# Optimization experiments

Hardware: AMD Instinct MI355X
Metric: run time of the kernel (lower is better)

The kernel has to match this reference:

```python
import jax, jax.numpy as jnp
import numpy as np
import math

D_MODEL = 1024
NUM_HEADS = 16
D_K = D_MODEL // NUM_HEADS
MAX_SEQ_LEN = 2048
THETA = 10000.0
BATCH = 2
SEQ = 2048


def setup_inputs() -> dict:
    key = jax.random.key(0)
    ks = jax.random.split(key, 5)
    std = math.sqrt(2.0 / (D_MODEL + D_MODEL))
    def w(k):
        return jnp.clip(std * jax.random.normal(k, (D_MODEL, D_MODEL), dtype=jnp.float32), -3 * std, 3 * std)
    return {
        "x": jax.random.normal(ks[0], (BATCH, SEQ, D_MODEL), dtype=jnp.float32),
        "token_positions": jnp.arange(SEQ, dtype=jnp.int32),
        "Wq": w(ks[1]),
        "Wk": w(ks[2]),
        "Wv": w(ks[3]),
        "Wo": w(ks[4]),
    }


def _rope_tables():
    inv_freq = 1.0 / THETA ** (jnp.arange(0, D_K, 2, dtype=jnp.float32) / D_K)  # [d_k/2]
    positions = jnp.arange(MAX_SEQ_LEN, dtype=jnp.float32)[:, None]             # [max_seq, 1]
    angles = positions * inv_freq                                               # [max_seq, d_k/2]
    return jnp.cos(angles), jnp.sin(angles)


def _apply_rope(x, cos, sin):
    # x: [..., seq, d_k]; cos/sin: [seq, d_k/2] (broadcast over leading dims)
    x1, x2 = x[..., ::2], x[..., 1::2]
    r1 = x1 * cos - x2 * sin
    r2 = x1 * sin + x2 * cos
    return jnp.stack((r1, r2), axis=-1).reshape(x.shape)


def reference(x, token_positions, Wq, Wk, Wv, Wo):
    B, S, D = x.shape
    def proj(W):
        y = jnp.einsum('bsd,od->bso', x, W)
        return y.reshape(B, S, NUM_HEADS, D_K).transpose(0, 2, 1, 3)  # [B,H,S,dk]
    q, k, v = proj(Wq), proj(Wk), proj(Wv)

    cos_t, sin_t = _rope_tables()
    cos, sin = cos_t[token_positions], sin_t[token_positions]  # [S, d_k/2]
    q = _apply_rope(q, cos, sin)
    k = _apply_rope(k, cos, sin)

    scores = jnp.einsum('bhqd,bhkd->bhqk', q, k) / math.sqrt(D_K)
    causal = jnp.tril(jnp.ones((S, S), dtype=bool))
    scores = jnp.where(causal, scores, -jnp.inf)
    attn = jax.nn.softmax(scores, axis=-1)
    out = jnp.einsum('bhqk,bhkd->bhqd', attn, v)
    out = out.transpose(0, 2, 1, 3).reshape(B, S, D)
    return jnp.einsum('bsd,od->bso', out, Wo)
```

## Files before the change

### kernel.cpp

```cpp
#include <hip/hip_runtime.h>
#include <hip/hip_bf16.h>


typedef __attribute__((ext_vector_type(8))) short short8;
typedef __attribute__((ext_vector_type(4))) float floatx4;

static __device__ __forceinline__ unsigned short f2bf(float f) {
  __hip_bfloat16 h = __float2bfloat16(f);
  return *(unsigned short*)&h;
}

static __device__ __forceinline__ unsigned int pk2bf(float a, float b) {
  unsigned int ua = __float_as_uint(a) + 0x8000u;
  unsigned int ub = __float_as_uint(b) + 0x8000u;
  return __builtin_amdgcn_perm(ub, ua, 0x07060302u);
}

static __device__ __forceinline__ float fexp2(float x) {
  float r;
  asm("v_exp_f32 %0, %1\n\ts_nop 0" : "=v"(r) : "v"(x));
  return r;
}

static __device__ __forceinline__ void gl2lds16(const unsigned short* g,
                                                unsigned short* l) {
  __builtin_amdgcn_global_load_lds(
      (const __attribute__((address_space(1))) void*)g,
      (__attribute__((address_space(3))) void*)l, 16, 0, 0);
}

__global__ __launch_bounds__(256) void cvt_all(
    const float4* __restrict__ x,  const float4* __restrict__ wq,
    const float4* __restrict__ wk, const float4* __restrict__ wv,
    const float4* __restrict__ wo,
    ushort4* __restrict__ xb,  ushort4* __restrict__ wqb,
    ushort4* __restrict__ wkb, ushort4* __restrict__ wvb,
    ushort4* __restrict__ wob,
    const int* __restrict__ tokpos,
    float* __restrict__ ctab, float* __restrict__ stab) {
  int t = blockIdx.y;
  int i = blockIdx.x * 256 + threadIdx.x;
  if (t == 5) {
    if (i < 65536) {
      int s = i >> 5, f = i & 31;
      float inv = expf(-9.210340371976184f * (float)(2 * f) / 64.0f);
      float ang = (float)tokpos[s] * inv;
      ctab[i] = cosf(ang);
      stab[i] = sinf(ang);
    }
    return;
  }
  const float4* s = (t == 0) ? x : (t == 1) ? wq : (t == 2) ? wk : (t == 3) ? wv : wo;
  ushort4* d = (t == 0) ? xb : (t == 1) ? wqb : (t == 2) ? wkb : (t == 3) ? wvb : wob;
  int n4 = (t == 0) ? 1048576 : 262144;
  if (i < n4) {
    float4 v = s[i];
    ushort4 o;
    o.x = f2bf(v.x); o.y = f2bf(v.y); o.z = f2bf(v.z); o.w = f2bf(v.w);
    d[i] = o;
  }
}

__global__ __launch_bounds__(256) void qkv_mfma(
    const unsigned short* __restrict__ X,
    const unsigned short* __restrict__ Wq,
    const unsigned short* __restrict__ Wk,
    const unsigned short* __restrict__ Wv,
    const float* __restrict__ ctab, const float* __restrict__ stab,
    unsigned short* __restrict__ Qo, unsigned short* __restrict__ Ko,
    unsigned short* __restrict__ Vo) {
  int mat = blockIdx.z;
  const unsigned short* W = (mat == 0) ? Wq : ((mat == 1) ? Wk : Wv);
  unsigned short* Out = (mat == 0) ? Qo : ((mat == 1) ? Ko : Vo);
  int t = blockIdx.x + (blockIdx.y << 6);
  int m0 = (t >> 3) * 64, n0 = (t & 7) * 128;

  __shared__ __align__(16) unsigned short lA[2][64 * 64];
  __shared__ __align__(16) unsigned short lB[2][128 * 64];
  int tid = threadIdx.x;
  int wave = tid >> 6, lane = tid & 63;
  int l15 = lane & 15, quad = lane >> 4;
  int rsub = lane >> 3, sch = lane & 7;
  int fsw = l15 & 7;

  floatx4 acc[4][2];
#pragma unroll
  for (int m = 0; m < 4; ++m)
#pragma unroll
    for (int n = 0; n < 2; ++n) acc[m][n] = (floatx4){0.f, 0.f, 0.f, 0.f};

#pragma unroll
  for (int kp = 0; kp < 2; ++kp) {
#pragma unroll
    for (int p = 0; p < 2; ++p) {
      int r = wave * 16 + p * 8 + rsub;
      int g = sch ^ (r & 7);
      gl2lds16(X + (size_t)(m0 + r) * 1024 + kp * 64 + g * 8,
               lA[kp] + (wave * 16 + p * 8) * 64);
    }
#pragma unroll
    for (int p = 0; p < 4; ++p) {
      int r = wave * 32 + p * 8 + rsub;
      int g = sch ^ (r & 7);
      gl2lds16(W + (size_t)(n0 + r) * 1024 + kp * 64 + g * 8,
               lB[kp] + (wave * 32 + p * 8) * 64);
    }
  }
  asm volatile("s_waitcnt vmcnt(6)" ::: "memory");
  __builtin_amdgcn_s_barrier();

  for (int kt = 0; kt < 16; ++kt) {
    int cur = kt & 1;
#pragma unroll
    for (int ks = 0; ks < 2; ++ks) {
      int slot = ((ks * 4 + quad) ^ fsw) * 8;
      short8 af[4], bf[2];
#pragma unroll
      for (int m = 0; m < 4; ++m)
        af[m] = *(const short8*)(lA[cur] + (m * 16 + l15) * 64 + slot);
#pragma unroll
      for (int n = 0; n < 2; ++n)
        bf[n] = *(const short8*)(lB[cur] + (wave * 32 + n * 16 + l15) * 64 + slot);
#pragma unroll
      for (int m = 0; m < 4; ++m)
#pragma unroll
        for (int n = 0; n < 2; ++n)
          acc[m][n] = __builtin_amdgcn_mfma_f32_16x16x32_bf16(
              af[m], bf[n], acc[m][n], 0, 0, 0);
    }
    if (kt == 15) break;
    __builtin_amdgcn_s_barrier();
    if (kt < 14) {
#pragma unroll
      for (int p = 0; p < 2; ++p) {
        int r = wave * 16 + p * 8 + rsub;
        int g = sch ^ (r & 7);
        gl2lds16(X + (size_t)(m0 + r) * 1024 + (kt + 2) * 64 + g * 8,
                 lA[cur] + (wave * 16 + p * 8) * 64);
      }
#pragma unroll
      for (int p = 0; p < 4; ++p) {
        int r = wave * 32 + p * 8 + rsub;
        int g = sch ^ (r & 7);
        gl2lds16(W + (size_t)(n0 + r) * 1024 + (kt + 2) * 64 + g * 8,
                 lB[cur] + (wave * 32 + p * 8) * 64);
      }
      asm volatile("s_waitcnt vmcnt(6)" ::: "memory");
    } else {
      asm volatile("s_waitcnt vmcnt(0)" ::: "memory");
    }
    __builtin_amdgcn_s_barrier();
  }

#pragma unroll
  for (int n = 0; n < 2; ++n) {
    int col = n0 + wave * 32 + n * 16 + l15;
    int h = col >> 6;
    int d = col & 63;
    int pi = d >> 1;
    bool odd = (d & 1) != 0;
    size_t hb = (size_t)h * 2048 * 64;
#pragma unroll
    for (int m = 0; m < 4; ++m) {
      int row0 = m0 + m * 16 + quad * 4;
      int b = row0 >> 11;
      int s0 = row0 & 2047;
      size_t base = (size_t)b * 16 * 2048 * 64 + hb;
      if (mat == 2) {
        ushort4 pv;
        pv.x = f2bf(acc[m][n][0]);
        pv.y = f2bf(acc[m][n][1]);
        pv.z = f2bf(acc[m][n][2]);
        pv.w = f2bf(acc[m][n][3]);
        *(ushort4*)(Out + base + (size_t)d * 2048 + s0) = pv;
      } else {
#pragma unroll
        for (int i = 0; i < 4; ++i) {
          int s = s0 + i;
          float v = acc[m][n][i];
          float p = __shfl_xor(v, 1);
          float c = ctab[s * 32 + pi];
          float sn = stab[s * 32 + pi];
          float res = odd ? fmaf(p, sn, v * c) : fmaf(v, c, -p * sn);
          if (mat == 0) res *= 0.1803368801111204f;
          Out[base + (size_t)s * 64 + d] = f2bf(res);
        }
      }
    }
  }
}

__global__ __launch_bounds__(256) void oproj_mfma(
    const unsigned short* __restrict__ A, const unsigned short* __restrict__ Wo,
    float* __restrict__ Out) {
  __shared__ __align__(16) unsigned short lA[2][64 * 64];
  __shared__ __align__(16) unsigned short lB[2][128 * 64];
  int tid = threadIdx.x;
  int wave = tid >> 6, lane = tid & 63;
  int l15 = lane & 15, quad = lane >> 4;
  int rsub = lane >> 3, sch = lane & 7;
  int fsw = l15 & 7;
  int t = blockIdx.x + (blockIdx.y << 6);
  int m0 = (t >> 3) * 64, n0 = (t & 7) * 128;

  floatx4 acc[4][2];
#pragma unroll
  for (int m = 0; m < 4; ++m)
#pragma unroll
    for (int n = 0; n < 2; ++n) acc[m][n] = (floatx4){0.f, 0.f, 0.f, 0.f};

#pragma unroll
  for (int kp = 0; kp < 2; ++kp) {
#pragma unroll
    for (int p = 0; p < 2; ++p) {
      int r = wave * 16 + p * 8 + rsub;
      int g = sch ^ (r & 7);
      gl2lds16(A + (size_t)(m0 + r) * 1024 + kp * 64 + g * 8,
               lA[kp] + (wave * 16 + p * 8) * 64);
    }
#pragma unroll
    for (int p = 0; p < 4; ++p) {
      int r = wave * 32 + p * 8 + rsub;
      int g = sch ^ (r & 7);
      gl2lds16(Wo + (size_t)(n0 + r) * 1024 + kp * 64 + g * 8,
               lB[kp] + (wave * 32 + p * 8) * 64);
    }
  }
  asm volatile("s_waitcnt vmcnt(6)" ::: "memory");
  __builtin_amdgcn_s_barrier();

  for (int kt = 0; kt < 16; ++kt) {
    int cur = kt & 1;
#pragma unroll
    for (int ks = 0; ks < 2; ++ks) {
      int slot = ((ks * 4 + quad) ^ fsw) * 8;
      short8 af[4], bf[2];
#pragma unroll
      for (int m = 0; m < 4; ++m)
        af[m] = *(const short8*)(lA[cur] + (m * 16 + l15) * 64 + slot);
#pragma unroll
      for (int n = 0; n < 2; ++n)
        bf[n] = *(const short8*)(lB[cur] + (wave * 32 + n * 16 + l15) * 64 + slot);
#pragma unroll
      for (int m = 0; m < 4; ++m)
#pragma unroll
        for (int n = 0; n < 2; ++n)
          acc[m][n] = __builtin_amdgcn_mfma_f32_16x16x32_bf16(
              af[m], bf[n], acc[m][n], 0, 0, 0);
    }
    if (kt == 15) break;
    __builtin_amdgcn_s_barrier();
    if (kt < 14) {
#pragma unroll
      for (int p = 0; p < 2; ++p) {
        int r = wave * 16 + p * 8 + rsub;
        int g = sch ^ (r & 7);
        gl2lds16(A + (size_t)(m0 + r) * 1024 + (kt + 2) * 64 + g * 8,
                 lA[cur] + (wave * 16 + p * 8) * 64);
      }
#pragma unroll
      for (int p = 0; p < 4; ++p) {
        int r = wave * 32 + p * 8 + rsub;
        int g = sch ^ (r & 7);
        gl2lds16(Wo + (size_t)(n0 + r) * 1024 + (kt + 2) * 64 + g * 8,
                 lB[cur] + (wave * 32 + p * 8) * 64);
      }
      asm volatile("s_waitcnt vmcnt(6)" ::: "memory");
    } else {
      asm volatile("s_waitcnt vmcnt(0)" ::: "memory");
    }
    __builtin_amdgcn_s_barrier();
  }

#pragma unroll
  for (int m = 0; m < 4; ++m) {
#pragma unroll
    for (int n = 0; n < 2; ++n) {
      int col = n0 + wave * 32 + n * 16 + l15;
#pragma unroll
      for (int i = 0; i < 4; ++i) {
        int row = m0 + m * 16 + quad * 4 + i;
        Out[(size_t)row * 1024 + col] = acc[m][n][i];
      }
    }
  }
}

static __device__ __forceinline__ void qk_step(
    const unsigned short* lK, int l15, int c0, int c1,
    short8 q0, short8 q1, floatx4 (&sc)[4]) {
#pragma unroll
  for (int sub = 0; sub < 4; ++sub) {
    const unsigned short* kr = lK + (sub * 16 + l15) * 64;
    short8 a0 = *(const short8*)(kr + c0);
    short8 a1 = *(const short8*)(kr + c1);
    floatx4 s = {0.f, 0.f, 0.f, 0.f};
    s = __builtin_amdgcn_mfma_f32_16x16x32_bf16(a0, q0, s, 0, 0, 0);
    s = __builtin_amdgcn_mfma_f32_16x16x32_bf16(a1, q1, s, 0, 0, 0);
    sc[sub] = s;
  }
}

static __device__ __forceinline__ void sm_step(
    floatx4 (&sc)[4], float& m_i, float& l_i, floatx4 (&o)[4],
    bool diag, int qin, int quad) {
  if (diag) {
#pragma unroll
    for (int sub = 0; sub < 4; ++sub)
#pragma unroll
      for (int i = 0; i < 4; ++i)
        if (sub * 16 + quad * 4 + i > qin) sc[sub][i] = -1e30f;
  }
  float mb = sc[0][0];
#pragma unroll
  for (int sub = 0; sub < 4; ++sub)
#pragma unroll
    for (int i = 0; i < 4; ++i) mb = fmaxf(mb, sc[sub][i]);
  mb = fmaxf(mb, __shfl_xor(mb, 16));
  mb = fmaxf(mb, __shfl_xor(mb, 32));

  if (!__all(mb <= m_i + 8.f)) {
    float mn = fmaxf(m_i, mb);
    float al = fexp2(m_i - mn);
    m_i = mn;
    l_i *= al;
#pragma unroll
    for (int n = 0; n < 4; ++n) {
      o[n][0] *= al; o[n][1] *= al; o[n][2] *= al; o[n][3] *= al;
    }
  }
  float rs = 0.f;
#pragma unroll
  for (int sub = 0; sub < 4; ++sub)
#pragma unroll
    for (int i = 0; i < 4; ++i) {
      float p = fexp2(sc[sub][i] - m_i);
      sc[sub][i] = p;
      rs += p;
    }
  rs += __shfl_xor(rs, 16);
  rs += __shfl_xor(rs, 32);
  l_i += rs;
}

static __device__ __forceinline__ void pv_step(
    const floatx4 (&sc)[4], floatx4 (&o)[4], unsigned short* lPws,
    const unsigned short* lV, int l15, int quad, int c0, int c1) {
  int swz = l15 & 7;
  unsigned short* pw = lPws + l15 * 64;
#pragma unroll
  for (int sub = 0; sub < 4; ++sub) {
    uint2 w;
    w.x = pk2bf(sc[sub][0], sc[sub][1]);
    w.y = pk2bf(sc[sub][2], sc[sub][3]);
    int slot = (sub * 2 + (quad >> 1)) ^ swz;
    *(uint2*)(pw + slot * 8 + (quad & 1) * 4) = w;
  }
  short8 pa0 = *(const short8*)(pw + ((quad ^ swz) * 8));
  short8 pa1 = *(const short8*)(pw + (((4 + quad) ^ swz) * 8));
#pragma unroll
  for (int n = 0; n < 4; ++n) {
    const unsigned short* vr = lV + (n * 16 + l15) * 64;
    short8 vb0 = *(const short8*)(vr + c0);
    short8 vb1 = *(const short8*)(vr + c1);
    o[n] = __builtin_amdgcn_mfma_f32_16x16x32_bf16(vb0, pa0, o[n], 0, 0, 0);
    o[n] = __builtin_amdgcn_mfma_f32_16x16x32_bf16(vb1, pa1, o[n], 0, 0, 0);
  }
}

__global__ __launch_bounds__(128, 2) void attn_flash(
    const unsigned short* __restrict__ Q, const unsigned short* __restrict__ K,
    const unsigned short* __restrict__ Vt, unsigned short* __restrict__ Oc) {
  __shared__ __align__(16) unsigned short lK[2][64 * 64];
  __shared__ __align__(16) unsigned short lV[2][64 * 64];
  __shared__ __align__(16) unsigned short lP[4][16 * 64];

  int tid = threadIdx.x;
  int wave = tid >> 6, lane = tid & 63;
  int l15 = lane & 15, quad = lane >> 4;

  int id = blockIdx.x;
  int bh = (id & 7) * 4 + ((id >> 3) & 3);
  int rem = id >> 5;
  int pair = rem >> 1;
  int h = rem & 1;
  int tA = pair, tB = 31 - pair;
  int NT = tB + 1;

  size_t base = (size_t)bh * 2048 * 64;
  int qoff = h * 32 + wave * 16 + l15;

  const unsigned short* qrowA = Q + base + (size_t)(tA * 64 + qoff) * 64;
  const unsigned short* qrowB = Q + base + (size_t)(tB * 64 + qoff) * 64;
  short8 qA0 = *(const short8*)(qrowA + quad * 8);
  short8 qA1 = *(const short8*)(qrowA + 32 + quad * 8);
  short8 qB0 = *(const short8*)(qrowB + quad * 8);
  short8 qB1 = *(const short8*)(qrowB + 32 + quad * 8);

  floatx4 oA[4], oB[4];
  float mA_i = -1e30f, lA_i = 0.f, mB_i = -1e30f, lB_i = 0.f;
#pragma unroll
  for (int n = 0; n < 4; ++n) {
    oA[n] = (floatx4){0.f, 0.f, 0.f, 0.f};
    oB[n] = (floatx4){0.f, 0.f, 0.f, 0.f};
  }

  int r0 = tid >> 3, g = tid & 7;
  int e0 = g * 8;
  int sl = (g ^ (r0 & 7)) * 8;
  int fsw = l15 & 7;
  int c0 = (quad ^ fsw) * 8;
  int c1 = ((quad + 4) ^ fsw) * 8;

  short8 pk0, pk1, pk2, pk3, pv0, pv1, pv2, pv3;

  {
    const unsigned short* kp = K + base;
    const unsigned short* vp = Vt + base;
    pk0 = *(const short8*)(kp + (r0 +  0) * 64 + e0);
    pk1 = *(const short8*)(kp + (r0 + 16) * 64 + e0);
    pk2 = *(const short8*)(kp + (r0 + 32) * 64 + e0);
    pk3 = *(const short8*)(kp + (r0 + 48) * 64 + e0);
    pv0 = *(const short8*)(vp + (size_t)(r0 +  0) * 2048 + e0);
    pv1 = *(const short8*)(vp + (size_t)(r0 + 16) * 2048 + e0);
    pv2 = *(const short8*)(vp + (size_t)(r0 + 32) * 2048 + e0);
    pv3 = *(const short8*)(vp + (size_t)(r0 + 48) * 2048 + e0);
  }
  *(short8*)(lK[0] + (r0 +  0) * 64 + sl) = pk0;
  *(short8*)(lK[0] + (r0 + 16) * 64 + sl) = pk1;
  *(short8*)(lK[0] + (r0 + 32) * 64 + sl) = pk2;
  *(short8*)(lK[0] + (r0 + 48) * 64 + sl) = pk3;
  *(short8*)(lV[0] + (r0 +  0) * 64 + sl) = pv0;
  *(short8*)(lV[0] + (r0 + 16) * 64 + sl) = pv1;
  *(short8*)(lV[0] + (r0 + 32) * 64 + sl) = pv2;
  *(short8*)(lV[0] + (r0 + 48) * 64 + sl) = pv3;
  {
    const unsigned short* kp = K + base + 4096;
    const unsigned short* vp = Vt + base + 64;
    pk0 = *(const short8*)(kp + (r0 +  0) * 64 + e0);
    pk1 = *(const short8*)(kp + (r0 + 16) * 64 + e0);
    pk2 = *(const short8*)(kp + (r0 + 32) * 64 + e0);
    pk3 = *(const short8*)(kp + (r0 + 48) * 64 + e0);
    pv0 = *(const short8*)(vp + (size_t)(r0 +  0) * 2048 + e0);
    pv1 = *(const short8*)(vp + (size_t)(r0 + 16) * 2048 + e0);
    pv2 = *(const short8*)(vp + (size_t)(r0 + 32) * 2048 + e0);
    pv3 = *(const short8*)(vp + (size_t)(r0 + 48) * 2048 + e0);
  }
  asm volatile("s_waitcnt lgkmcnt(0)" ::: "memory");
  __builtin_amdgcn_s_barrier();
  __builtin_amdgcn_sched_barrier(0);

  int qin = qoff;

  for (int kt = 0; kt < NT; ++kt) {
    int cur = kt & 1;
    bool aAct = (kt <= tA);
    const unsigned short* lKc = lK[cur];
    const unsigned short* lVc = lV[cur];

    floatx4 scB[4], scA[4];
    qk_step(lKc, l15, c0, c1, qB0, qB1, scB);
    if (aAct) qk_step(lKc, l15, c0, c1, qA0, qA1, scA);

    sm_step(scB, mB_i, lB_i, oB, kt == NT - 1, qin, quad);
    if (aAct) sm_step(scA, mA_i, lA_i, oA, kt == tA, qin, quad);

    pv_step(scB, oB, lP[wave * 2], lVc, l15, quad, c0, c1);
    if (aAct) pv_step(scA, oA, lP[wave * 2 + 1], lVc, l15, quad, c0, c1);

    if (kt + 1 < NT) {
      unsigned short* wK = lK[cur ^ 1];
      unsigned short* wV = lV[cur ^ 1];
      *(short8*)(wK + (r0 +  0) * 64 + sl) = pk0;
      *(short8*)(wK + (r0 + 16) * 64 + sl) = pk1;
      *(short8*)(wK + (r0 + 32) * 64 + sl) = pk2;
      *(short8*)(wK + (r0 + 48) * 64 + sl) = pk3;
      *(short8*)(wV + (r0 +  0) * 64 + sl) = pv0;
      *(short8*)(wV + (r0 + 16) * 64 + sl) = pv1;
      *(short8*)(wV + (r0 + 32) * 64 + sl) = pv2;
      *(short8*)(wV + (r0 + 48) * 64 + sl) = pv3;
      if (kt + 2 < NT) {
        const unsigned short* kp = K + base + (size_t)(kt + 2) * 4096;
        const unsigned short* vp = Vt + base + (size_t)(kt + 2) * 64;
        pk0 = *(const short8*)(kp + (r0 +  0) * 64 + e0);
        pk1 = *(const short8*)(kp + (r0 + 16) * 64 + e0);
        pk2 = *(const short8*)(kp + (r0 + 32) * 64 + e0);
        pk3 = *(const short8*)(kp + (r0 + 48) * 64 + e0);
        pv0 = *(const short8*)(vp + (size_t)(r0 +  0) * 2048 + e0);
        pv1 = *(const short8*)(vp + (size_t)(r0 + 16) * 2048 + e0);
        pv2 = *(const short8*)(vp + (size_t)(r0 + 32) * 2048 + e0);
        pv3 = *(const short8*)(vp + (size_t)(r0 + 48) * 2048 + e0);
      }
      asm volatile("s_waitcnt lgkmcnt(0)" ::: "memory");
      __builtin_amdgcn_s_barrier();
      __builtin_amdgcn_sched_barrier(0);
    }
  }

  int b = bh >> 4, hh = bh & 15;
  {
    float inv = 1.f / lB_i;
    int s = tB * 64 + qoff;
    size_t orow = (size_t)(b * 2048 + s) * 1024 + hh * 64;
#pragma unroll
    for (int n = 0; n < 4; ++n) {
      uint2 ov;
      ov.x = pk2bf(oB[n][0] * inv, oB[n][1] * inv);
      ov.y = pk2bf(oB[n][2] * inv, oB[n][3] * inv);
      *(uint2*)(Oc + orow + n * 16 + quad * 4) = ov;
    }
  }
  {
    float inv = 1.f / lA_i;
    int s = tA * 64 + qoff;
    size_t orow = (size_t)(b * 2048 + s) * 1024 + hh * 64;
#pragma unroll
    for (int n = 0; n < 4; ++n) {
      uint2 ov;
      ov.x = pk2bf(oA[n][0] * inv, oA[n][1] * inv);
      ov.y = pk2bf(oA[n][2] * inv, oA[n][3] * inv);
      *(uint2*)(Oc + orow + n * 16 + quad * 4) = ov;
    }
  }
}

extern "C" void kernel_launch(void* const* d_in, const int* in_sizes, int n_in,
                              void* d_out, int out_size, void* d_ws, size_t ws_size,
                              hipStream_t stream) {
  const float* x  = (const float*)d_in[0];
  const int* tokpos = (const int*)d_in[1];
  const float* Wq = (const float*)d_in[2];
  const float* Wk = (const float*)d_in[3];
  const float* Wv = (const float*)d_in[4];
  const float* Wo = (const float*)d_in[5];
  float* out = (float*)d_out;

  float* ws = (float*)d_ws;
  float* ctab = ws;
  float* stab = ctab + 65536;
  unsigned short* u = (unsigned short*)(stab + 65536);
  unsigned short* Qb  = u;
  unsigned short* Kb  = Qb + 4194304;
  unsigned short* Vb  = Kb + 4194304;
  unsigned short* Oc  = Vb + 4194304;
  unsigned short* xb  = Oc + 4194304;
  unsigned short* Wqb = xb + 4194304;
  unsigned short* Wkb = Wqb + 1048576;
  unsigned short* Wvb = Wkb + 1048576;
  unsigned short* Wob = Wvb + 1048576;

  cvt_all<<<dim3(4096, 6), 256, 0, stream>>>(
      (const float4*)x, (const float4*)Wq, (const float4*)Wk,
      (const float4*)Wv, (const float4*)Wo,
      (ushort4*)xb, (ushort4*)Wqb, (ushort4*)Wkb, (ushort4*)Wvb, (ushort4*)Wob,
      tokpos, ctab, stab);

  qkv_mfma<<<dim3(64, 8, 3), 256, 0, stream>>>(
      xb, Wqb, Wkb, Wvb, ctab, stab, Qb, Kb, Vb);
  attn_flash<<<dim3(1024), 128, 0, stream>>>(Qb, Kb, Vb, Oc);
  oproj_mfma<<<dim3(64, 8), 256, 0, stream>>>(Oc, Wob, out);
}
```

Baseline: 181.0 us.

## Merge attention block halves into one 256-thread block sharing K/V tiles

The flash attention kernel now launches 512 blocks of 4 waves, each covering a full 64-row query tile pair. Before, 1024 blocks of 2 waves each handled half the rows and each loaded the same K/V tiles. Sharing K/V tiles across four waves halves global-to-LDS staging traffic per query row and cuts per-thread prefetch registers. The max and sum reductions in the softmax step are also rewritten as trees to shorten dependency chains. The cost is half as many blocks for load balancing, more LDS for P buffers, and larger barrier groups.

```diff
diff --git a/kernel.cpp b/kernel.cpp
--- a/kernel.cpp
+++ b/kernel.cpp
@@ -311,11 +311,11 @@
       for (int i = 0; i < 4; ++i)
         if (sub * 16 + quad * 4 + i > qin) sc[sub][i] = -1e30f;
   }
-  float mb = sc[0][0];
-#pragma unroll
-  for (int sub = 0; sub < 4; ++sub)
-#pragma unroll
-    for (int i = 0; i < 4; ++i) mb = fmaxf(mb, sc[sub][i]);
+  float t0 = fmaxf(fmaxf(sc[0][0], sc[0][1]), fmaxf(sc[0][2], sc[0][3]));
+  float t1 = fmaxf(fmaxf(sc[1][0], sc[1][1]), fmaxf(sc[1][2], sc[1][3]));
+  float t2 = fmaxf(fmaxf(sc[2][0], sc[2][1]), fmaxf(sc[2][2], sc[2][3]));
+  float t3 = fmaxf(fmaxf(sc[3][0], sc[3][1]), fmaxf(sc[3][2], sc[3][3]));
+  float mb = fmaxf(fmaxf(t0, t1), fmaxf(t2, t3));
   mb = fmaxf(mb, __shfl_xor(mb, 16));
   mb = fmaxf(mb, __shfl_xor(mb, 32));
 
@@ -329,15 +329,16 @@
       o[n][0] *= al; o[n][1] *= al; o[n][2] *= al; o[n][3] *= al;
     }
   }
-  float rs = 0.f;
 #pragma unroll
   for (int sub = 0; sub < 4; ++sub)
 #pragma unroll
-    for (int i = 0; i < 4; ++i) {
-      float p = fexp2(sc[sub][i] - m_i);
-      sc[sub][i] = p;
-      rs += p;
-    }
+    for (int i = 0; i < 4; ++i)
+      sc[sub][i] = fexp2(sc[sub][i] - m_i);
+  float s0 = (sc[0][0] + sc[0][1]) + (sc[0][2] + sc[0][3]);
+  float s1 = (sc[1][0] + sc[1][1]) + (sc[1][2] + sc[1][3]);
+  float s2 = (sc[2][0] + sc[2][1]) + (sc[2][2] + sc[2][3]);
+  float s3 = (sc[3][0] + sc[3][1]) + (sc[3][2] + sc[3][3]);
+  float rs = (s0 + s1) + (s2 + s3);
   rs += __shfl_xor(rs, 16);
   rs += __shfl_xor(rs, 32);
   l_i += rs;
@@ -368,12 +369,12 @@
   }
 }
 
-__global__ __launch_bounds__(128, 2) void attn_flash(
+__global__ __launch_bounds__(256, 3) void attn_flash(
     const unsigned short* __restrict__ Q, const unsigned short* __restrict__ K,
     const unsigned short* __restrict__ Vt, unsigned short* __restrict__ Oc) {
   __shared__ __align__(16) unsigned short lK[2][64 * 64];
   __shared__ __align__(16) unsigned short lV[2][64 * 64];
-  __shared__ __align__(16) unsigned short lP[4][16 * 64];
+  __shared__ __align__(16) unsigned short lP[8][16 * 64];
 
   int tid = threadIdx.x;
   int wave = tid >> 6, lane = tid & 63;
@@ -381,14 +382,12 @@
 
   int id = blockIdx.x;
   int bh = (id & 7) * 4 + ((id >> 3) & 3);
-  int rem = id >> 5;
-  int pair = rem >> 1;
-  int h = rem & 1;
+  int pair = id >> 5;
   int tA = pair, tB = 31 - pair;
   int NT = tB + 1;
 
   size_t base = (size_t)bh * 2048 * 64;
-  int qoff = h * 32 + wave * 16 + l15;
+  int qoff = wave * 16 + l15;
 
   const unsigned short* qrowA = Q + base + (size_t)(tA * 64 + qoff) * 64;
   const unsigned short* qrowB = Q + base + (size_t)(tB * 64 + qoff) * 64;
@@ -406,45 +405,34 @@
   }
 
   int r0 = tid >> 3, g = tid & 7;
+  int r1 = r0 + 32;
   int e0 = g * 8;
   int sl = (g ^ (r0 & 7)) * 8;
   int fsw = l15 & 7;
   int c0 = (quad ^ fsw) * 8;
   int c1 = ((quad + 4) ^ fsw) * 8;
 
-  short8 pk0, pk1, pk2, pk3, pv0, pv1, pv2, pv3;
+  short8 pk0, pk1, pv0, pv1;
 
   {
     const unsigned short* kp = K + base;
     const unsigned short* vp = Vt + base;
-    pk0 = *(const short8*)(kp + (r0 +  0) * 64 + e0);
-    pk1 = *(const short8*)(kp + (r0 + 16) * 64 + e0);
-    pk2 = *(const short8*)(kp + (r0 + 32) * 64 + e0);
-    pk3 = *(const short8*)(kp + (r0 + 48) * 64 + e0);
-    pv0 = *(const short8*)(vp + (size_t)(r0 +  0) * 2048 + e0);
-    pv1 = *(const short8*)(vp + (size_t)(r0 + 16) * 2048 + e0);
-    pv2 = *(const short8*)(vp + (size_t)(r0 + 32) * 2048 + e0);
-    pv3 = *(const short8*)(vp + (size_t)(r0 + 48) * 2048 + e0);
-  }
-  *(short8*)(lK[0] + (r0 +  0) * 64 + sl) = pk0;
-  *(short8*)(lK[0] + (r0 + 16) * 64 + sl) = pk1;
-  *(short8*)(lK[0] + (r0 + 32) * 64 + sl) = pk2;
-  *(short8*)(lK[0] + (r0 + 48) * 64 + sl) = pk3;
-  *(short8*)(lV[0] + (r0 +  0) * 64 + sl) = pv0;
-  *(short8*)(lV[0] + (r0 + 16) * 64 + sl) = pv1;
-  *(short8*)(lV[0] + (r0 + 32) * 64 + sl) = pv2;
-  *(short8*)(lV[0] + (r0 + 48) * 64 + sl) = pv3;
+    pk0 = *(const short8*)(kp + r0 * 64 + e0);
+    pk1 = *(const short8*)(kp + r1 * 64 + e0);
+    pv0 = *(const short8*)(vp + (size_t)r0 * 2048 + e0);
+    pv1 = *(const short8*)(vp + (size_t)r1 * 2048 + e0);
+  }
+  *(short8*)(lK[0] + r0 * 64 + sl) = pk0;
+  *(short8*)(lK[0] + r1 * 64 + sl) = pk1;
+  *(short8*)(lV[0] + r0 * 64 + sl) = pv0;
+  *(short8*)(lV[0] + r1 * 64 + sl) = pv1;
   {
     const unsigned short* kp = K + base + 4096;
     const unsigned short* vp = Vt + base + 64;
-    pk0 = *(const short8*)(kp + (r0 +  0) * 64 + e0);
-    pk1 = *(const short8*)(kp + (r0 + 16) * 64 + e0);
-    pk2 = *(const short8*)(kp + (r0 + 32) * 64 + e0);
-    pk3 = *(const short8*)(kp + (r0 + 48) * 64 + e0);
-    pv0 = *(const short8*)(vp + (size_t)(r0 +  0) * 2048 + e0);
-    pv1 = *(const short8*)(vp + (size_t)(r0 + 16) * 2048 + e0);
-    pv2 = *(const short8*)(vp + (size_t)(r0 + 32) * 2048 + e0);
-    pv3 = *(const short8*)(vp + (size_t)(r0 + 48) * 2048 + e0);
+    pk0 = *(const short8*)(kp + r0 * 64 + e0);
+    pk1 = *(const short8*)(kp + r1 * 64 + e0);
+    pv0 = *(const short8*)(vp + (size_t)r0 * 2048 + e0);
+    pv1 = *(const short8*)(vp + (size_t)r1 * 2048 + e0);
   }
   asm volatile("s_waitcnt lgkmcnt(0)" ::: "memory");
   __builtin_amdgcn_s_barrier();
@@ -471,25 +459,17 @@
     if (kt + 1 < NT) {
       unsigned short* wK = lK[cur ^ 1];
       unsigned short* wV = lV[cur ^ 1];
-      *(short8*)(wK + (r0 +  0) * 64 + sl) = pk0;
-      *(short8*)(wK + (r0 + 16) * 64 + sl) = pk1;
-      *(short8*)(wK + (r0 + 32) * 64 + sl) = pk2;
-      *(short8*)(wK + (r0 + 48) * 64 + sl) = pk3;
-      *(short8*)(wV + (r0 +  0) * 64 + sl) = pv0;
-      *(short8*)(wV + (r0 + 16) * 64 + sl) = pv1;
-      *(short8*)(wV + (r0 + 32) * 64 + sl) = pv2;
-      *(short8*)(wV + (r0 + 48) * 64 + sl) = pv3;
+      *(short8*)(wK + r0 * 64 + sl) = pk0;
+      *(short8*)(wK + r1 * 64 + sl) = pk1;
+      *(short8*)(wV + r0 * 64 + sl) = pv0;
+      *(short8*)(wV + r1 * 64 + sl) = pv1;
       if (kt + 2 < NT) {
         const unsigned short* kp = K + base + (size_t)(kt + 2) * 4096;
         const unsigned short* vp = Vt + base + (size_t)(kt + 2) * 64;
-        pk0 = *(const short8*)(kp + (r0 +  0) * 64 + e0);
-        pk1 = *(const short8*)(kp + (r0 + 16) * 64 + e0);
-        pk2 = *(const short8*)(kp + (r0 + 32) * 64 + e0);
-        pk3 = *(const short8*)(kp + (r0 + 48) * 64 + e0);
-        pv0 = *(const short8*)(vp + (size_t)(r0 +  0) * 2048 + e0);
-        pv1 = *(const short8*)(vp + (size_t)(r0 + 16) * 2048 + e0);
-        pv2 = *(const short8*)(vp + (size_t)(r0 + 32) * 2048 + e0);
-        pv3 = *(const short8*)(vp + (size_t)(r0 + 48) * 2048 + e0);
+        pk0 = *(const short8*)(kp + r0 * 64 + e0);
+        pk1 = *(const short8*)(kp + r1 * 64 + e0);
+        pv0 = *(const short8*)(vp + (size_t)r0 * 2048 + e0);
+        pv1 = *(const short8*)(vp + (size_t)r1 * 2048 + e0);
       }
       asm volatile("s_waitcnt lgkmcnt(0)" ::: "memory");
       __builtin_amdgcn_s_barrier();
@@ -557,6 +537,6 @@
 
   qkv_mfma<<<dim3(64, 8, 3), 256, 0, stream>>>(
       xb, Wqb, Wkb, Wvb, ctab, stab, Qb, Kb, Vb);
-  attn_flash<<<dim3(1024), 128, 0, stream>>>(Qb, Kb, Vb, Oc);
+  attn_flash<<<dim3(512), 256, 0, stream>>>(Qb, Kb, Vb, Oc);
   oproj_mfma<<<dim3(64, 8), 256, 0, stream>>>(Oc, Wob, out);
 }
```

After: 179.8 us. No clear change (-0.6%).
